# Optimization experiments

Hardware: AMD Instinct MI355X
Metric: run time of the kernel (lower is better)

The kernel has to match this reference:

```python
import jax, jax.numpy as jnp
import numpy as np

B, N, G = 4096, 20, 4
D_IN, D_OUT, H = 128, 64, 8
LRELU = 0.2  # TF leaky_relu default alpha


def _glorot(key, shape):
    fan_in, fan_out = shape[-2], shape[-1]
    scale = jnp.sqrt(6.0 / (fan_in + fan_out)).astype(jnp.float32)
    return jax.random.uniform(key, shape, jnp.float32, -1.0, 1.0) * scale


def setup_inputs() -> dict:
    key = jax.random.key(0)
    k1, k2, k3, k4, k5, k6 = jax.random.split(key, 6)
    return {
        "self_vecs": jax.random.normal(k1, (B, G, D_IN), jnp.float32),
        "neigh_vecs": jax.random.normal(k2, (B, N, G, D_IN), jnp.float32),
        "W_heads": _glorot(k3, (H, D_IN, D_OUT)),      # per-head before_attend_weights
        "a_self": _glorot(k4, (H, D_OUT, 1))[..., 0],  # per-head attend_weights_self  [H, D_OUT]
        "a_neigh": _glorot(k5, (H, D_OUT, 1))[..., 0], # per-head attend_weights_neigh [H, D_OUT]
        "W_out": _glorot(k6, (H * D_OUT, D_OUT)),      # final FC weights
    }


def reference(self_vecs, neigh_vecs, W_heads, a_self, a_neigh, W_out):
    # Transform self and neighbor vectors for all heads at once.
    self_t = jnp.einsum("bgd,hde->bghe", self_vecs, W_heads)    # [B,G,H,E]
    neigh_t = jnp.einsum("bngd,hde->bnghe", neigh_vecs, W_heads)  # [B,N,G,H,E]

    f_self = jnp.einsum("bghe,he->bgh", self_t, a_self)          # [B,G,H]
    f_neigh = jnp.einsum("bnghe,he->bngh", neigh_t, a_neigh)     # [B,N,G,H]

    # logits [B,N,G,H]; original applies softmax over the num_graphs axis (tf default last axis of [B,N,G])
    logits = f_self[:, None, :, :] + f_neigh
    attend = jax.nn.softmax(jax.nn.leaky_relu(logits, LRELU), axis=2)  # softmax over G

    # Weighted aggregation over neighbors: [B,G,H,E]
    out_h = jnp.einsum("bngh,bnghe->bghe", attend, neigh_t)
    out_h = jax.nn.leaky_relu(out_h, LRELU)  # per-head activation (act=leaky_relu)

    # Concatenate heads along feature dim -> [B,G,H*E], final FC + relu
    h = out_h.reshape(out_h.shape[0], out_h.shape[1], H * D_OUT)
    return jax.nn.relu(jnp.einsum("bgk,ke->bge", h, W_out))
```

## Files before the change

kernel.cpp:

```cpp
#include <hip/hip_runtime.h>
#include <hip/hip_bf16.h>

#define BB 4096
#define NNB 20
#define GG 4
#define DIN 128
#define EE 64
#define HH 8

typedef short bf16x8 __attribute__((ext_vector_type(8)));
typedef float f32x4 __attribute__((ext_vector_type(4)));

__device__ __forceinline__ float lrelu_f(float x) { return x > 0.f ? x : 0.2f * x; }
__device__ __forceinline__ unsigned short f2bf(float f) {
  unsigned u = __float_as_uint(f);
  return (unsigned short)((u + 0x7fffu + ((u >> 16) & 1u)) >> 16);
}
__device__ __forceinline__ float bf2f(unsigned short s) {
  return __uint_as_float(((unsigned)s) << 16);
}

__global__ __launch_bounds__(256) void prep_kernel(
    const float* __restrict__ W_heads, const float* __restrict__ a_self,
    const float* __restrict__ a_neigh, const float* __restrict__ W_out,
    unsigned short* __restrict__ P1Whi, unsigned short* __restrict__ P1Wlo,
    unsigned short* __restrict__ WBhi, unsigned short* __restrict__ WBlo,
    unsigned short* __restrict__ WOhi, unsigned short* __restrict__ WOlo) {
  int id = blockIdx.x * 256 + threadIdx.x;
  if (id < 2048) {
    int j = id & 7, lane = (id >> 3) & 63, kb = id >> 9;
    int col = lane & 15, k = kb * 32 + (lane >> 4) * 8 + j;
    int h = col & 7;
    const float* a = (col < 8) ? a_neigh : a_self;
    const float* Wrow = W_heads + (h * DIN + k) * EE;
    float acc = 0.f;
    for (int e = 0; e < EE; ++e) acc = fmaf(Wrow[e], a[h * EE + e], acc);
    unsigned short hi = f2bf(acc);
    P1Whi[id] = hi;
    P1Wlo[id] = f2bf(acc - bf2f(hi));
  } else if (id < 2048 + 65536) {
    int rel = id - 2048;
    int j = rel & 7, l = (rel >> 3) & 63, kb = (rel >> 9) & 3, nt = (rel >> 11) & 3, h = rel >> 13;
    int d = kb * 32 + (l >> 4) * 8 + j;
    int e = nt * 16 + (l & 15);
    float w = W_heads[(h * DIN + d) * EE + e];
    unsigned short hi = f2bf(w);
    WBhi[rel] = hi;
    WBlo[rel] = f2bf(w - bf2f(hi));
  } else if (id < 2048 + 65536 + 32768) {
    int rel = id - 2048 - 65536;
    int j = rel & 7, l = (rel >> 3) & 63, kb = (rel >> 9) & 15, nt = rel >> 13;
    int k = kb * 32 + (l >> 4) * 8 + j;
    int n = nt * 16 + (l & 15);
    float w = W_out[k * EE + n];
    unsigned short hi = f2bf(w);
    WOhi[rel] = hi;
    WOlo[rel] = f2bf(w - bf2f(hi));
  }
}

__global__ __launch_bounds__(512, 4) void fused_kernel(
    const float* __restrict__ self_vecs, const float* __restrict__ neigh_vecs,
    const unsigned short* __restrict__ P1Whi, const unsigned short* __restrict__ P1Wlo,
    const unsigned short* __restrict__ WBhi, const unsigned short* __restrict__ WBlo,
    const unsigned short* __restrict__ WOhi, const unsigned short* __restrict__ WOlo,
    float* __restrict__ out) {
  __shared__ char smem[57344];
  char* aggb = smem;
  float* attw = (float*)(smem + 32768);
  char* hb = smem + 32768;

  const int t = threadIdx.x;
  const int w = t >> 6, lane = t & 63;
  const int m = lane & 15, kg = lane >> 4;
  const int bid = blockIdx.x;

  bf16x8 wfh[4], wfl[4];
#pragma unroll
  for (int kb = 0; kb < 4; ++kb) {
    wfh[kb] = *(const bf16x8*)(P1Whi + (kb * 64 + lane) * 8);
    wfl[kb] = *(const bf16x8*)(P1Wlo + (kb * 64 + lane) * 8);
  }

#define P1_TILE(rowp, cvec)                                                    \
  {                                                                            \
    _Pragma("unroll") for (int kb = 0; kb < 4; ++kb) {                         \
      float4 xa = *(const float4*)((rowp) + kb * 32 + kg * 8);                 \
      float4 xb = *(const float4*)((rowp) + kb * 32 + kg * 8 + 4);             \
      float xv[8] = {xa.x, xa.y, xa.z, xa.w, xb.x, xb.y, xb.z, xb.w};          \
      bf16x8 xh, xl;                                                           \
      _Pragma("unroll") for (int j = 0; j < 8; ++j) {                          \
        unsigned short hi = f2bf(xv[j]);                                       \
        xh[j] = (short)hi;                                                     \
        xl[j] = (short)f2bf(xv[j] - bf2f(hi));                                 \
      }                                                                        \
      cvec = __builtin_amdgcn_mfma_f32_16x16x32_bf16(xh, wfh[kb], cvec, 0, 0, 0); \
      cvec = __builtin_amdgcn_mfma_f32_16x16x32_bf16(xh, wfl[kb], cvec, 0, 0, 0); \
      cvec = __builtin_amdgcn_mfma_f32_16x16x32_bf16(xl, wfh[kb], cvec, 0, 0, 0); \
    }                                                                          \
  }

#define P1_SOFTMAX(tile, cvec)                                                 \
  if (m < 8) {                                                                 \
    float l[4], mx = -1e30f;                                                   \
    _Pragma("unroll") for (int gg = 0; gg < 4; ++gg) {                         \
      float v = lrelu_f(fs[gg] + (cvec)[gg]);                                  \
      l[gg] = v;                                                               \
      mx = fmaxf(mx, v);                                                       \
    }                                                                          \
    float s = 0.f;                                                             \
    _Pragma("unroll") for (int gg = 0; gg < 4; ++gg) {                         \
      l[gg] = __expf(l[gg] - mx);                                              \
      s += l[gg];                                                              \
    }                                                                          \
    float inv = 1.f / s;                                                       \
    _Pragma("unroll") for (int gg = 0; gg < 4; ++gg)                           \
      attw[(tile) * 128 + (kg * 4 + gg) * 8 + m] = l[gg] * inv;                \
  }

  f32x4 fs;
  {
    f32x4 c20 = {0.f, 0.f, 0.f, 0.f};
    const float* srow = self_vecs + ((size_t)bid * 16 + m) * DIN;
    P1_TILE(srow, c20)
#pragma unroll
    for (int reg = 0; reg < 4; ++reg) fs[reg] = __shfl_xor(c20[reg], 8);
  }

  const int bl_m = m >> 2, g_m = m & 3;
  const float* base_n =
      neigh_vecs + ((size_t)(bid * 4 + bl_m) * NNB * GG + g_m) * DIN;
  {
    f32x4 cA = {0.f, 0.f, 0.f, 0.f}, cB = {0.f, 0.f, 0.f, 0.f};
    const float* rpA = base_n + (size_t)w * (GG * DIN);
    const float* rpB = base_n + (size_t)(w + 8) * (GG * DIN);
    P1_TILE(rpA, cA)
    P1_TILE(rpB, cB)
    if (w < 4) {
      f32x4 cC = {0.f, 0.f, 0.f, 0.f};
      const float* rpC = base_n + (size_t)(w + 16) * (GG * DIN);
      P1_TILE(rpC, cC)
      P1_SOFTMAX(w + 16, cC)
    }
    P1_SOFTMAX(w, cA)
    P1_SOFTMAX(w + 8, cB)
  }
  __syncthreads();

#pragma unroll
  for (int i = 0; i < 2; ++i) {
    const int bg = 2 * w + i;
    const int bl = bg >> 2, g = bg & 3;
    const float* nbw = neigh_vecs + ((size_t)(bid * 4 + bl) * NNB * GG + g) * DIN;
    float acc[8][2];
#pragma unroll
    for (int h = 0; h < 8; ++h) { acc[h][0] = 0.f; acc[h][1] = 0.f; }
#pragma unroll
    for (int n = 0; n < NNB; ++n) {
      float2 x2 = *(const float2*)&nbw[(size_t)n * GG * DIN + 2 * lane];
      f32x4 a0 = *(const f32x4*)&attw[n * 128 + bg * 8];
      f32x4 a1 = *(const f32x4*)&attw[n * 128 + bg * 8 + 4];
#pragma unroll
      for (int h = 0; h < 4; ++h) {
        acc[h][0] = fmaf(a0[h], x2.x, acc[h][0]);
        acc[h][1] = fmaf(a0[h], x2.y, acc[h][1]);
        acc[h + 4][0] = fmaf(a1[h], x2.x, acc[h + 4][0]);
        acc[h + 4][1] = fmaf(a1[h], x2.y, acc[h + 4][1]);
      }
    }
    const int swz = (bg & 7) << 4;
#pragma unroll
    for (int h = 0; h < 8; ++h) {
      unsigned pack = (unsigned)f2bf(acc[h][0]) | ((unsigned)f2bf(acc[h][1]) << 16);
      *(unsigned*)(aggb + ((bg * 2048 + h * 256 + 4 * lane) ^ swz)) = pack;
    }
  }
  __syncthreads();

  {
    const int hh = w;
    const int aswz = (m & 7) << 4;
    bf16x8 a[4];
#pragma unroll
    for (int kb = 0; kb < 4; ++kb)
      a[kb] = *(const bf16x8*)(aggb + ((m * 2048 + hh * 256 + kb * 64 + kg * 16) ^ aswz));
#pragma unroll
    for (int nt = 0; nt < 4; ++nt) {
      f32x4 c = {0.f, 0.f, 0.f, 0.f};
#pragma unroll
      for (int kb = 0; kb < 4; ++kb) {
        const int fi = (((hh * 4 + nt) * 4 + kb) * 64 + lane) * 8;
        bf16x8 bh = *(const bf16x8*)(WBhi + fi);
        bf16x8 bl_ = *(const bf16x8*)(WBlo + fi);
        c = __builtin_amdgcn_mfma_f32_16x16x32_bf16(a[kb], bh, c, 0, 0, 0);
        c = __builtin_amdgcn_mfma_f32_16x16x32_bf16(a[kb], bl_, c, 0, 0, 0);
      }
      const int k = hh * 64 + nt * 16 + m;
#pragma unroll
      for (int reg = 0; reg < 4; ++reg) {
        int row = kg * 4 + reg;
        int byte = (row * 1024 + k * 2) ^ ((row & 7) << 4);
        *(unsigned short*)(hb + byte) = f2bf(lrelu_f(c[reg]));
      }
    }
  }
  __syncthreads();

  if (w < 4) {
    const int nt = w;
    f32x4 acc = {0.f, 0.f, 0.f, 0.f};
    for (int kb = 0; kb < 16; ++kb) {
      int byte = (m * 1024 + (kb * 32 + kg * 8) * 2) ^ ((m & 7) << 4);
      bf16x8 ah = *(const bf16x8*)(hb + byte);
      const int fi = ((nt * 16 + kb) * 64 + lane) * 8;
      bf16x8 bh = *(const bf16x8*)(WOhi + fi);
      bf16x8 bl_ = *(const bf16x8*)(WOlo + fi);
      acc = __builtin_amdgcn_mfma_f32_16x16x32_bf16(ah, bh, acc, 0, 0, 0);
      acc = __builtin_amdgcn_mfma_f32_16x16x32_bf16(ah, bl_, acc, 0, 0, 0);
    }
    const int rbase = bid * 16;
#pragma unroll
    for (int reg = 0; reg < 4; ++reg) {
      int row = rbase + kg * 4 + reg;
      out[(size_t)row * EE + nt * 16 + m] = fmaxf(acc[reg], 0.f);
    }
  }
#undef P1_TILE
#undef P1_SOFTMAX
}

extern "C" void kernel_launch(void* const* d_in, const int* in_sizes, int n_in,
                              void* d_out, int out_size, void* d_ws, size_t ws_size,
                              hipStream_t stream) {
  (void)in_sizes; (void)n_in; (void)out_size; (void)ws_size;
  const float* self_vecs  = (const float*)d_in[0];
  const float* neigh_vecs = (const float*)d_in[1];
  const float* W_heads    = (const float*)d_in[2];
  const float* a_self     = (const float*)d_in[3];
  const float* a_neigh    = (const float*)d_in[4];
  const float* W_out      = (const float*)d_in[5];
  float* out              = (float*)d_out;

  char* ws = (char*)d_ws;
  unsigned short* P1Whi = (unsigned short*)ws;
  unsigned short* P1Wlo = (unsigned short*)(ws + 4096);
  unsigned short* WBhi  = (unsigned short*)(ws + 8192);
  unsigned short* WBlo  = (unsigned short*)(ws + 8192 + 131072);
  unsigned short* WOhi  = (unsigned short*)(ws + 8192 + 262144);
  unsigned short* WOlo  = (unsigned short*)(ws + 8192 + 262144 + 65536);

  prep_kernel<<<(2048 + 65536 + 32768) / 256, 256, 0, stream>>>(
      W_heads, a_self, a_neigh, W_out, P1Whi, P1Wlo, WBhi, WBlo, WOhi, WOlo);

  fused_kernel<<<BB / 4, 512, 0, stream>>>(
      self_vecs, neigh_vecs, P1Whi, P1Wlo, WBhi, WBlo, WOhi, WOlo, out);
}
```

Measured before the change: 72.06 us.

## Stage phase-1 weights in LDS and prefetch input tiles ahead of MFMA

Result: no change. 71.37 us (-1.0%).

```diff
diff --git a/kernel.cpp b/kernel.cpp
--- a/kernel.cpp
+++ b/kernel.cpp
@@ -75,28 +75,32 @@
   const int m = lane & 15, kg = lane >> 4;
   const int bid = blockIdx.x;
 
-  bf16x8 wfh[4], wfl[4];
-#pragma unroll
-  for (int kb = 0; kb < 4; ++kb) {
-    wfh[kb] = *(const bf16x8*)(P1Whi + (kb * 64 + lane) * 8);
-    wfl[kb] = *(const bf16x8*)(P1Wlo + (kb * 64 + lane) * 8);
-  }
-
-#define P1_TILE(rowp, cvec)                                                    \
+#define LOAD_X(X, ptr)                                                         \
+  {                                                                            \
+    const float4* p_ = (const float4*)(ptr);                                   \
+    _Pragma("unroll") for (int q = 0; q < 4; ++q) {                            \
+      X[2 * q]     = p_[q * 8 + kg * 2];                                       \
+      X[2 * q + 1] = p_[q * 8 + kg * 2 + 1];                                   \
+    }                                                                          \
+  }
+
+#define PROC_TILE(X, cvec)                                                     \
   {                                                                            \
     _Pragma("unroll") for (int kb = 0; kb < 4; ++kb) {                         \
-      float4 xa = *(const float4*)((rowp) + kb * 32 + kg * 8);                 \
-      float4 xb = *(const float4*)((rowp) + kb * 32 + kg * 8 + 4);             \
-      float xv[8] = {xa.x, xa.y, xa.z, xa.w, xb.x, xb.y, xb.z, xb.w};          \
+      float xv[8] = {X[2 * kb].x,     X[2 * kb].y,     X[2 * kb].z,            \
+                     X[2 * kb].w,     X[2 * kb + 1].x, X[2 * kb + 1].y,        \
+                     X[2 * kb + 1].z, X[2 * kb + 1].w};                        \
       bf16x8 xh, xl;                                                           \
       _Pragma("unroll") for (int j = 0; j < 8; ++j) {                          \
         unsigned short hi = f2bf(xv[j]);                                       \
         xh[j] = (short)hi;                                                     \
         xl[j] = (short)f2bf(xv[j] - bf2f(hi));                                 \
       }                                                                        \
-      cvec = __builtin_amdgcn_mfma_f32_16x16x32_bf16(xh, wfh[kb], cvec, 0, 0, 0); \
-      cvec = __builtin_amdgcn_mfma_f32_16x16x32_bf16(xh, wfl[kb], cvec, 0, 0, 0); \
-      cvec = __builtin_amdgcn_mfma_f32_16x16x32_bf16(xl, wfh[kb], cvec, 0, 0, 0); \
+      bf16x8 wh = *(const bf16x8*)(smem + kb * 1024 + lane * 16);              \
+      bf16x8 wl = *(const bf16x8*)(smem + 4096 + kb * 1024 + lane * 16);       \
+      cvec = __builtin_amdgcn_mfma_f32_16x16x32_bf16(xh, wh, cvec, 0, 0, 0);   \
+      cvec = __builtin_amdgcn_mfma_f32_16x16x32_bf16(xh, wl, cvec, 0, 0, 0);   \
+      cvec = __builtin_amdgcn_mfma_f32_16x16x32_bf16(xl, wh, cvec, 0, 0, 0);   \
     }                                                                          \
   }
 
@@ -118,33 +122,40 @@
       attw[(tile) * 128 + (kg * 4 + gg) * 8 + m] = l[gg] * inv;                \
   }
 
+  const int bl_m = m >> 2, g_m = m & 3;
+  const float* base_n =
+      neigh_vecs + ((size_t)(bid * 4 + bl_m) * NNB * GG + g_m) * DIN;
+
+  float4 XS[8], XA[8], XB[8], XC[8];
+  LOAD_X(XS, self_vecs + ((size_t)bid * 16 + m) * DIN)
+  LOAD_X(XA, base_n + (size_t)w * (GG * DIN))
+
+  {
+    const float4* src = (t < 256) ? (const float4*)P1Whi : (const float4*)P1Wlo;
+    ((float4*)smem)[t] = src[t & 255];
+  }
+  __syncthreads();
+
   f32x4 fs;
   {
     f32x4 c20 = {0.f, 0.f, 0.f, 0.f};
-    const float* srow = self_vecs + ((size_t)bid * 16 + m) * DIN;
-    P1_TILE(srow, c20)
+    PROC_TILE(XS, c20)
 #pragma unroll
     for (int reg = 0; reg < 4; ++reg) fs[reg] = __shfl_xor(c20[reg], 8);
   }
-
-  const int bl_m = m >> 2, g_m = m & 3;
-  const float* base_n =
-      neigh_vecs + ((size_t)(bid * 4 + bl_m) * NNB * GG + g_m) * DIN;
-  {
-    f32x4 cA = {0.f, 0.f, 0.f, 0.f}, cB = {0.f, 0.f, 0.f, 0.f};
-    const float* rpA = base_n + (size_t)w * (GG * DIN);
-    const float* rpB = base_n + (size_t)(w + 8) * (GG * DIN);
-    P1_TILE(rpA, cA)
-    P1_TILE(rpB, cB)
-    if (w < 4) {
-      f32x4 cC = {0.f, 0.f, 0.f, 0.f};
-      const float* rpC = base_n + (size_t)(w + 16) * (GG * DIN);
-      P1_TILE(rpC, cC)
-      P1_SOFTMAX(w + 16, cC)
-    }
-    P1_SOFTMAX(w, cA)
-    P1_SOFTMAX(w + 8, cB)
-  }
+  LOAD_X(XB, base_n + (size_t)(w + 8) * (GG * DIN))
+
+  f32x4 cA = {0.f, 0.f, 0.f, 0.f}, cB = {0.f, 0.f, 0.f, 0.f};
+  PROC_TILE(XA, cA)
+  if (w < 4) LOAD_X(XC, base_n + (size_t)(w + 16) * (GG * DIN))
+  PROC_TILE(XB, cB)
+  if (w < 4) {
+    f32x4 cC = {0.f, 0.f, 0.f, 0.f};
+    PROC_TILE(XC, cC)
+    P1_SOFTMAX(w + 16, cC)
+  }
+  P1_SOFTMAX(w, cA)
+  P1_SOFTMAX(w + 8, cB)
   __syncthreads();
 
 #pragma unroll
@@ -225,7 +236,8 @@
       out[(size_t)row * EE + nt * 16 + m] = fmaxf(acc[reg], 0.f);
     }
   }
-#undef P1_TILE
+#undef LOAD_X
+#undef PROC_TILE
 #undef P1_SOFTMAX
 }
 
```
